# Performance work log

Hardware: AMD Instinct MI355X
Metric: run time of the kernel (lower is better)

Reference implementation:

```python
import jax, jax.numpy as jnp
import numpy as np

B, C, T, F_ = 4, 128, 1000, 65
H, E, Dh = 4, 8, 32          # E = ceil(512/65), Dh = C // H
POOL, STRIDE = 10, 5
EPS = 1e-5


def setup_inputs() -> dict:
    key = jax.random.key(0)
    ks = jax.random.split(key, 16)
    s = 0.05
    d = {}
    d['batch'] = jax.random.normal(ks[0], (B, C, T, F_), jnp.float32)
    d['pos_cond'] = jax.random.normal(ks[1], (B, C, T, F_), jnp.float32)
    d['neg_cond'] = jax.random.normal(ks[2], (B, C, T, F_), jnp.float32)
    # per-head 1x1 conv params (stacked over heads), PReLU slopes, LN4DCF affine
    d['WQ'] = jax.random.normal(ks[3], (H, E, C), jnp.float32) * s
    d['bQ'] = jax.random.normal(ks[4], (H, E), jnp.float32) * s
    d['aQ'] = jnp.full((H,), 0.25, jnp.float32)
    d['gQ'] = jnp.ones((H, E, F_), jnp.float32)
    d['betQ'] = jnp.zeros((H, E, F_), jnp.float32)
    d['WK'] = jax.random.normal(ks[5], (H, E, C), jnp.float32) * s
    d['bK'] = jax.random.normal(ks[6], (H, E), jnp.float32) * s
    d['aK'] = jnp.full((H,), 0.25, jnp.float32)
    d['gK'] = jnp.ones((H, E, F_), jnp.float32)
    d['betK'] = jnp.zeros((H, E, F_), jnp.float32)
    d['WV'] = jax.random.normal(ks[7], (H, Dh, C), jnp.float32) * s
    d['bV'] = jax.random.normal(ks[8], (H, Dh), jnp.float32) * s
    d['aV'] = jnp.full((H,), 0.25, jnp.float32)
    d['gV'] = jnp.ones((H, Dh, F_), jnp.float32)
    d['betV'] = jnp.zeros((H, Dh, F_), jnp.float32)
    d['Wp'] = jax.random.normal(ks[9], (C, C), jnp.float32) * s
    d['bp'] = jax.random.normal(ks[10], (C,), jnp.float32) * s
    d['ap'] = jnp.full((1,), 0.25, jnp.float32)
    d['gp'] = jnp.ones((C, F_), jnp.float32)
    d['betp'] = jnp.zeros((C, F_), jnp.float32)
    return d


def _avg_pool_time(x):
    # x: [B, C, T, F] -> pool along T (torch pools after transposing to [.., F, T])
    xt = jnp.transpose(x, (0, 1, 3, 2))  # [B, C, F, T]
    y = jax.lax.reduce_window(xt, 0.0, jax.lax.add,
                              (1, 1, 1, POOL), (1, 1, 1, STRIDE), 'VALID') / POOL
    return jnp.transpose(y, (0, 1, 3, 2))  # [B, C, T', F]


def _head_branch(x, W, b, a, g, bet):
    # x: [B, Cin, Tx, F]; W: [H, Co, Cin] -> y: [H, B, Co, Tx, F]
    y = jnp.einsum('bctf,hec->hbetf', x, W) + b[:, None, :, None, None]
    y = jnp.where(y >= 0, y, a[:, None, None, None, None] * y)  # PReLU
    mu = jnp.mean(y, axis=(2, 4), keepdims=True)                 # LN over (C, F)
    var = jnp.var(y, axis=(2, 4), keepdims=True)
    return (y - mu) / jnp.sqrt(var + EPS) * g[:, None, :, None, :] + bet[:, None, :, None, :]


def reference(batch, pos_cond, neg_cond,
              WQ, bQ, aQ, gQ, betQ,
              WK, bK, aK, gK, betK,
              WV, bV, aV, gV, betV,
              Wp, bp, ap, gp, betp):
    cond = jnp.concatenate([_avg_pool_time(pos_cond), -_avg_pool_time(neg_cond)], axis=2)
    Tc = cond.shape[2]

    Q = _head_branch(batch, WQ, bQ, aQ, gQ, betQ)   # [H,B,E,T,F]
    K = _head_branch(cond, WK, bK, aK, gK, betK)    # [H,B,E,Tc,F]
    V = _head_branch(cond, WV, bV, aV, gV, betV)    # [H,B,Dh,Tc,F]

    Qf = jnp.transpose(Q, (0, 1, 3, 2, 4)).reshape(H, B, T, E * F_)
    Kf = jnp.transpose(K, (0, 1, 3, 2, 4)).reshape(H, B, Tc, E * F_)
    Vf = jnp.transpose(V, (0, 1, 3, 2, 4)).reshape(H, B, Tc, Dh * F_)

    scale = 1.0 / jnp.sqrt(jnp.float32(E * F_))
    attn = jax.nn.softmax(jnp.einsum('hbtd,hbsd->hbts', Qf, Kf) * scale, axis=-1)
    out = jnp.einsum('hbts,hbse->hbte', attn, Vf)   # [H,B,T,Dh*F]

    out = out.reshape(H, B, T, Dh, F_)
    out = jnp.transpose(out, (1, 0, 3, 2, 4)).reshape(B, C, T, F_)

    # concat projection: conv1x1 + PReLU + LN4DCF over (C, F)
    y = jnp.einsum('bctf,ec->betf', out, Wp) + bp[None, :, None, None]
    y = jnp.where(y >= 0, y, ap[0] * y)
    mu = jnp.mean(y, axis=(1, 3), keepdims=True)
    var = jnp.var(y, axis=(1, 3), keepdims=True)
    y = (y - mu) / jnp.sqrt(var + EPS) * gp[None, :, None, :] + betp[None, :, None, :]
    return y
```

## Files before the change

### kernel.cpp

```cpp
#include <hip/hip_runtime.h>
#include <hip/hip_bf16.h>

typedef unsigned short u16;
typedef __attribute__((ext_vector_type(8))) short bfrag;
typedef __attribute__((ext_vector_type(4))) float f32x4;

#define B_ 4
#define C_ 128
#define T_ 1000
#define F_ 65
#define H_ 4
#define E_ 8
#define DH_ 32
#define TP_ 199
#define TC_ 398
#define DQK 520
#define DQKP 544
#define DV 2080
#define SP_ 416
#define QROWS 1008
#define EPS 1e-5f

__device__ __forceinline__ float bf2f(u16 u) {
    union { float f; unsigned int i; } v; v.i = ((unsigned int)u) << 16; return v.f;
}
__device__ __forceinline__ u16 f2bf(float f) {
    union { float f; unsigned int i; } v; v.f = f;
    unsigned int x = v.i;
    return (u16)((x + 0x7FFFu + ((x >> 16) & 1u)) >> 16);
}

__device__ __forceinline__ float ldx(const float* p, int i) { return p[i]; }
__device__ __forceinline__ float ldx(const u16* p, int i) { return bf2f(p[i]); }

__device__ __forceinline__ float wred_sum(float v) {
#pragma unroll
    for (int o = 32; o > 0; o >>= 1) v += __shfl_down(v, o, 64);
    return __shfl(v, 0, 64);
}

__global__ __launch_bounds__(256)
void pool_kernel(const float* __restrict__ pos, const float* __restrict__ neg,
                 u16* __restrict__ cond) {
    int idx = blockIdx.x * 256 + threadIdx.x;
    const int N = B_ * C_ * TC_ * F_;
    if (idx >= N) return;
    int f  = idx % F_;
    int tc = (idx / F_) % TC_;
    int c  = (idx / (F_ * TC_)) % C_;
    int b  = idx / (F_ * TC_ * C_);
    const float* src; float sign; int t0;
    if (tc < TP_) { src = pos; sign =  1.f; t0 = tc * 5; }
    else          { src = neg; sign = -1.f; t0 = (tc - TP_) * 5; }
    int base = ((b * C_ + c) * T_ + t0) * F_ + f;
    float s = 0.f;
#pragma unroll
    for (int k = 0; k < 10; k++) s += src[base + k * F_];
    cond[idx] = f2bf(s * (sign * 0.1f));
}

template <typename XT>
__global__ __launch_bounds__(256)
void qk_branch_kernel(const XT* __restrict__ x, int Tx, int rowsper, int ldout,
                      const float* __restrict__ W, const float* __restrict__ bias,
                      const float* __restrict__ alpha,
                      const float* __restrict__ g, const float* __restrict__ bet,
                      u16* __restrict__ out) {
    __shared__ float xs[C_ * F_ + 8];
    int b = blockIdx.x / Tx, t = blockIdx.x % Tx;
    int tid = threadIdx.x;
    int xbase = (b * C_) * Tx * F_ + t * F_;
    for (int i = tid; i < C_ * F_; i += 256) {
        int c = i / F_, f = i % F_;
        xs[i] = ldx(x, xbase + c * Tx * F_ + f);
    }
    if (tid < 8) xs[C_ * F_ + tid] = 0.f;
    __syncthreads();

    int row = tid >> 3;
    int oct = tid & 7;
    int h = row >> 3;
    float acc[9];
    float bb = bias[row];
#pragma unroll
    for (int j = 0; j < 9; j++) acc[j] = bb;
    for (int c = 0; c < C_; c++) {
        float w = W[row * C_ + c];
        const float* xr = &xs[c * F_ + oct];
#pragma unroll
        for (int j = 0; j < 9; j++) acc[j] = fmaf(w, xr[8 * j], acc[j]);
    }
    float a = alpha[h];
    float sum = 0.f, ss = 0.f;
#pragma unroll
    for (int j = 0; j < 9; j++) {
        int f = oct + 8 * j;
        if (f < F_) {
            float v = acc[j];
            v = (v >= 0.f) ? v : a * v;
            acc[j] = v;
            sum += v; ss += v * v;
        }
    }
    sum = wred_sum(sum); ss = wred_sum(ss);
    float mu = sum * (1.f / 520.f);
    float var = ss * (1.f / 520.f) - mu * mu;
    float rs = rsqrtf(var + EPS);
    size_t obase = (size_t)((h * B_ + b) * rowsper + t) * ldout + (row & 7) * F_;
#pragma unroll
    for (int j = 0; j < 9; j++) {
        int f = oct + 8 * j;
        if (f < F_) {
            float gv = g[row * F_ + f];
            float bv = bet[row * F_ + f];
            out[obase + f] = f2bf((acc[j] - mu) * rs * gv + bv);
        }
    }
}

__global__ __launch_bounds__(256)
void v_branch_kernel(const u16* __restrict__ x,
                     const float* __restrict__ W, const float* __restrict__ bias,
                     const float* __restrict__ alpha,
                     const float* __restrict__ g, const float* __restrict__ bet,
                     u16* __restrict__ out) {
    __shared__ float xs[C_ * F_ + 1];
    int b = blockIdx.x / TC_, t = blockIdx.x % TC_;
    int tid = threadIdx.x;
    int xbase = (b * C_) * TC_ * F_ + t * F_;
    for (int i = tid; i < C_ * F_; i += 256) {
        int c = i / F_, f = i % F_;
        xs[i] = bf2f(x[xbase + c * TC_ * F_ + f]);
    }
    if (tid == 0) xs[C_ * F_] = 0.f;
    __syncthreads();

    int row = tid >> 1;
    int half = tid & 1;
    int h = row >> 5;
    int f0 = half ? 33 : 0;
    float acc[33];
    float bb = bias[row];
#pragma unroll
    for (int j = 0; j < 33; j++) acc[j] = bb;
    for (int c = 0; c < C_; c++) {
        float w = W[row * C_ + c];
        const float* xr = &xs[c * F_ + f0];
#pragma unroll
        for (int j = 0; j < 33; j++) acc[j] = fmaf(w, xr[j], acc[j]);
    }
    float a = alpha[h];
    float sum = 0.f, ss = 0.f;
#pragma unroll
    for (int j = 0; j < 33; j++) {
        if (f0 + j < F_) {
            float v = acc[j];
            v = (v >= 0.f) ? v : a * v;
            acc[j] = v;
            sum += v; ss += v * v;
        }
    }
    sum = wred_sum(sum); ss = wred_sum(ss);
    float mu = sum * (1.f / 2080.f);
    float var = ss * (1.f / 2080.f) - mu * mu;
    float rs = rsqrtf(var + EPS);
    size_t obase = (size_t)((h * B_ + b) * TC_ + t) * DV + (row & 31) * F_ + f0;
#pragma unroll
    for (int j = 0; j < 33; j++) {
        if (f0 + j < F_) {
            float gv = g[row * F_ + f0 + j];
            float bv = bet[row * F_ + f0 + j];
            out[obase + j] = f2bf((acc[j] - mu) * rs * gv + bv);
        }
    }
}

__global__ __launch_bounds__(256)
void transpose_v_kernel(const u16* __restrict__ Vf, u16* __restrict__ Vt) {
    __shared__ u16 tileb[32][33];
    int id = blockIdx.x;
    int sb = id % 13; id /= 13;
    int eb = id % 65; int hb = id / 65;
    const u16* src = Vf + (size_t)hb * TC_ * DV;
    u16* dst = Vt + (size_t)hb * DV * SP_;
    int j = threadIdx.x & 31, i0 = threadIdx.x >> 5;
#pragma unroll
    for (int k = 0; k < 4; k++) {
        int i = i0 + 8 * k;
        int s = sb * 32 + i, e = eb * 32 + j;
        u16 v = 0;
        if (s < TC_) v = src[(size_t)s * DV + e];
        tileb[i][j] = v;
    }
    __syncthreads();
#pragma unroll
    for (int k = 0; k < 4; k++) {
        int i2 = i0 + 8 * k;
        int e = eb * 32 + i2, s = sb * 32 + j;
        dst[(size_t)e * SP_ + s] = tileb[j][i2];
    }
}

__global__ __launch_bounds__(256, 4)
void attn_kernel(const u16* __restrict__ Qf, const u16* __restrict__ Kf,
                 const u16* __restrict__ Vt, float* __restrict__ out) {
    __shared__ u16 qlds[16 * 552];
    __shared__ u16 plds[16 * 424];
    __shared__ float redmax[16 * 4];
    __shared__ float redsum[16 * 4];

    int tile = blockIdx.x % 63;
    int hb   = blockIdx.x / 63;
    int h = hb >> 2, b = hb & 3;
    int tid = threadIdx.x;
    int wave = tid >> 6, lane = tid & 63;
    int g = lane >> 4;
    int n = lane & 15;
    int tq0 = tile * 16;

    const u16* qbase = Qf + (size_t)(hb * QROWS + tq0) * DQK;
    for (int i = tid; i < 16 * 69; i += 256) {
        int q = i / 69, cb = i % 69;
        uint4 val = make_uint4(0, 0, 0, 0);
        if (cb < 65) val = *(const uint4*)(qbase + (size_t)q * DQK + cb * 8);
        *(uint4*)(&qlds[q * 552 + cb * 8]) = val;
    }
    __syncthreads();

    f32x4 acc[7];
#pragma unroll
    for (int i = 0; i < 7; i++) acc[i] = (f32x4){0.f, 0.f, 0.f, 0.f};
    const u16* kslab = Kf + (size_t)hb * SP_ * DQKP;
    for (int c = 0; c < 17; c++) {
        bfrag aq = *(const bfrag*)(&qlds[n * 552 + c * 32 + g * 8]);
#pragma unroll
        for (int i = 0; i < 7; i++) {
            int tau = wave + 4 * i;
            if (tau < 26) {
                bfrag bk = *(const bfrag*)(kslab + (size_t)(tau * 16 + n) * DQKP + c * 32 + g * 8);
                acc[i] = __builtin_amdgcn_mfma_f32_16x16x32_bf16(aq, bk, acc[i], 0, 0, 0);
            }
        }
    }

    const float scale = 0.043852900965f;
    float m4[4], s4[4];
#pragma unroll
    for (int r = 0; r < 4; r++) {
        float mx = -1e30f;
#pragma unroll
        for (int i = 0; i < 7; i++) {
            int tau = wave + 4 * i;
            int s = tau * 16 + n;
            if (tau < 26 && s < TC_) mx = fmaxf(mx, acc[i][r] * scale);
        }
        mx = fmaxf(mx, __shfl_xor(mx, 1, 64));
        mx = fmaxf(mx, __shfl_xor(mx, 2, 64));
        mx = fmaxf(mx, __shfl_xor(mx, 4, 64));
        mx = fmaxf(mx, __shfl_xor(mx, 8, 64));
        m4[r] = mx;
    }
    if (n == 0) {
#pragma unroll
        for (int r = 0; r < 4; r++) redmax[(g * 4 + r) * 4 + wave] = m4[r];
    }
    __syncthreads();
#pragma unroll
    for (int r = 0; r < 4; r++) {
        int q = g * 4 + r;
        m4[r] = fmaxf(fmaxf(redmax[q * 4 + 0], redmax[q * 4 + 1]),
                      fmaxf(redmax[q * 4 + 2], redmax[q * 4 + 3]));
        s4[r] = 0.f;
    }
#pragma unroll
    for (int i = 0; i < 7; i++) {
        int tau = wave + 4 * i;
        if (tau < 26) {
            int s = tau * 16 + n;
#pragma unroll
            for (int r = 0; r < 4; r++) {
                float e = (s < TC_) ? __expf(acc[i][r] * scale - m4[r]) : 0.f;
                acc[i][r] = e;
                s4[r] += e;
            }
        }
    }
#pragma unroll
    for (int r = 0; r < 4; r++) {
        float sm = s4[r];
        sm += __shfl_xor(sm, 1, 64);
        sm += __shfl_xor(sm, 2, 64);
        sm += __shfl_xor(sm, 4, 64);
        sm += __shfl_xor(sm, 8, 64);
        s4[r] = sm;
    }
    if (n == 0) {
#pragma unroll
        for (int r = 0; r < 4; r++) redsum[(g * 4 + r) * 4 + wave] = s4[r];
    }
    __syncthreads();
#pragma unroll
    for (int r = 0; r < 4; r++) {
        int q = g * 4 + r;
        float tot = redsum[q * 4 + 0] + redsum[q * 4 + 1] + redsum[q * 4 + 2] + redsum[q * 4 + 3];
        s4[r] = 1.0f / tot;
    }
#pragma unroll
    for (int i = 0; i < 7; i++) {
        int tau = wave + 4 * i;
        if (tau < 26) {
            int s = tau * 16 + n;
#pragma unroll
            for (int r = 0; r < 4; r++) {
                plds[(g * 4 + r) * 424 + s] = f2bf(acc[i][r] * s4[r]);
            }
        }
    }
    __syncthreads();

    bfrag bp[13];
#pragma unroll
    for (int c = 0; c < 13; c++)
        bp[c] = *(const bfrag*)(&plds[n * 424 + c * 32 + g * 8]);

    const u16* vslab = Vt + (size_t)hb * DV * SP_;
    int t = tq0 + n;
    for (int j = 0; j < 17; j++) {
        int p = wave + 4 * j;
        if (p >= 65) break;
        int e0 = p * 32;
        f32x4 a0 = (f32x4){0.f, 0.f, 0.f, 0.f};
        f32x4 a1 = (f32x4){0.f, 0.f, 0.f, 0.f};
#pragma unroll
        for (int c = 0; c < 13; c++) {
            bfrag v0 = *(const bfrag*)(vslab + (size_t)(e0 + n) * SP_ + c * 32 + g * 8);
            bfrag v1 = *(const bfrag*)(vslab + (size_t)(e0 + 16 + n) * SP_ + c * 32 + g * 8);
            a0 = __builtin_amdgcn_mfma_f32_16x16x32_bf16(v0, bp[c], a0, 0, 0, 0);
            a1 = __builtin_amdgcn_mfma_f32_16x16x32_bf16(v1, bp[c], a1, 0, 0, 0);
        }
        if (t < T_) {
#pragma unroll
            for (int r = 0; r < 4; r++) {
                int e = e0 + g * 4 + r;
                int dh = e / F_, f = e - dh * F_;
                out[((size_t)(b * C_ + h * DH_ + dh) * T_ + t) * F_ + f] = a0[r];
                int e2 = e0 + 16 + g * 4 + r;
                int dh2 = e2 / F_, f2 = e2 - dh2 * F_;
                out[((size_t)(b * C_ + h * DH_ + dh2) * T_ + t) * F_ + f2] = a1[r];
            }
        }
    }
}

__global__ __launch_bounds__(256)
void wconv_kernel(const float* __restrict__ W, u16* __restrict__ Wbf) {
    int i = blockIdx.x * 256 + threadIdx.x;
    if (i < C_ * C_) Wbf[i] = f2bf(W[i]);
}

__global__ __launch_bounds__(256, 4)
void proj_mfma_kernel(float* __restrict__ io, const u16* __restrict__ Wbf,
                      const float* __restrict__ bpr, const float* __restrict__ apr,
                      const float* __restrict__ gpr, const float* __restrict__ betpr) {
    __shared__ u16 xt[80 * 136];
    __shared__ float wsum[4], wss[4];
    int b = blockIdx.x / T_, t = blockIdx.x % T_;
    int tid = threadIdx.x;
    size_t xbase = (size_t)(b * C_) * T_ * F_ + (size_t)t * F_;

    for (int i = tid; i < C_ * F_; i += 256) {
        int c = i / F_, f = i % F_;
        xt[f * 136 + c] = f2bf(io[xbase + (size_t)c * T_ * F_ + f]);
    }
    for (int i = tid; i < 15 * 128; i += 256) {
        int f = 65 + i / 128, c = i % 128;
        xt[f * 136 + c] = 0;
    }
    __syncthreads();

    int wave = tid >> 6, lane = tid & 63, g = lane >> 4, n = lane & 15;
    f32x4 acc[2][5];
#pragma unroll
    for (int a = 0; a < 2; a++)
#pragma unroll
        for (int ft = 0; ft < 5; ft++) acc[a][ft] = (f32x4){0.f, 0.f, 0.f, 0.f};

    for (int c32 = 0; c32 < 4; c32++) {
        bfrag aw0 = *(const bfrag*)(Wbf + (size_t)(wave * 32 + n) * C_ + c32 * 32 + g * 8);
        bfrag aw1 = *(const bfrag*)(Wbf + (size_t)(wave * 32 + 16 + n) * C_ + c32 * 32 + g * 8);
#pragma unroll
        for (int ft = 0; ft < 5; ft++) {
            bfrag bx = *(const bfrag*)(&xt[(ft * 16 + n) * 136 + c32 * 32 + g * 8]);
            acc[0][ft] = __builtin_amdgcn_mfma_f32_16x16x32_bf16(aw0, bx, acc[0][ft], 0, 0, 0);
            acc[1][ft] = __builtin_amdgcn_mfma_f32_16x16x32_bf16(aw1, bx, acc[1][ft], 0, 0, 0);
        }
    }

    float a_p = apr[0];
    float sum = 0.f, ss = 0.f;
#pragma unroll
    for (int a = 0; a < 2; a++) {
        int e0 = wave * 32 + a * 16 + g * 4;
#pragma unroll
        for (int r = 0; r < 4; r++) {
            float bb = bpr[e0 + r];
#pragma unroll
            for (int ft = 0; ft < 5; ft++) {
                float v = acc[a][ft][r] + bb;
                v = (v >= 0.f) ? v : a_p * v;
                acc[a][ft][r] = v;
                int f = ft * 16 + n;
                if (f < F_) { sum += v; ss += v * v; }
            }
        }
    }
    sum = wred_sum(sum); ss = wred_sum(ss);
    if (lane == 0) { wsum[wave] = sum; wss[wave] = ss; }
    __syncthreads();
    float tsum = wsum[0] + wsum[1] + wsum[2] + wsum[3];
    float tss  = wss[0] + wss[1] + wss[2] + wss[3];
    float mu = tsum * (1.f / 8320.f);
    float var = tss * (1.f / 8320.f) - mu * mu;
    float rs = rsqrtf(var + EPS);

#pragma unroll
    for (int a = 0; a < 2; a++) {
#pragma unroll
        for (int r = 0; r < 4; r++) {
            int e = wave * 32 + a * 16 + g * 4 + r;
#pragma unroll
            for (int ft = 0; ft < 5; ft++) {
                int f = ft * 16 + n;
                if (f < F_) {
                    io[((size_t)(b * C_ + e) * T_ + t) * F_ + f] =
                        (acc[a][ft][r] - mu) * rs * gpr[e * F_ + f] + betpr[e * F_ + f];
                }
            }
        }
    }
}

extern "C" void kernel_launch(void* const* d_in, const int* in_sizes, int n_in,
                              void* d_out, int out_size, void* d_ws, size_t ws_size,
                              hipStream_t stream) {
    const float* batch = (const float*)d_in[0];
    const float* pos   = (const float*)d_in[1];
    const float* neg   = (const float*)d_in[2];
    const float* WQ   = (const float*)d_in[3];
    const float* bQ   = (const float*)d_in[4];
    const float* aQ   = (const float*)d_in[5];
    const float* gQ   = (const float*)d_in[6];
    const float* betQ = (const float*)d_in[7];
    const float* WK   = (const float*)d_in[8];
    const float* bK   = (const float*)d_in[9];
    const float* aK   = (const float*)d_in[10];
    const float* gK   = (const float*)d_in[11];
    const float* betK = (const float*)d_in[12];
    const float* WV   = (const float*)d_in[13];
    const float* bV   = (const float*)d_in[14];
    const float* aV   = (const float*)d_in[15];
    const float* gV   = (const float*)d_in[16];
    const float* betV = (const float*)d_in[17];
    const float* Wp   = (const float*)d_in[18];
    const float* bp   = (const float*)d_in[19];
    const float* ap   = (const float*)d_in[20];
    const float* gp   = (const float*)d_in[21];
    const float* betp = (const float*)d_in[22];

    char* ws = (char*)d_ws;
    u16* Vt   = (u16*)(ws);
    u16* cond = (u16*)(ws);
    u16* Qf   = (u16*)(ws + 27688960);
    u16* Kf   = (u16*)(ws + 44462080);
    u16* Vf   = (u16*)(ws + 51703808);
    u16* Wbf  = (u16*)(ws + 51703808);
    float* o  = (float*)d_out;

    const int NPOOL = B_ * C_ * TC_ * F_;
    pool_kernel<<<(NPOOL + 255) / 256, 256, 0, stream>>>(pos, neg, cond);
    qk_branch_kernel<float><<<B_ * T_,  256, 0, stream>>>(batch, T_,  QROWS, DQK,  WQ, bQ, aQ, gQ, betQ, Qf);
    qk_branch_kernel<u16>  <<<B_ * TC_, 256, 0, stream>>>(cond,  TC_, SP_,   DQKP, WK, bK, aK, gK, betK, Kf);
    v_branch_kernel <<<B_ * TC_, 256, 0, stream>>>(cond, WV, bV, aV, gV, betV, Vf);
    transpose_v_kernel<<<16 * 65 * 13, 256, 0, stream>>>(Vf, Vt);
    wconv_kernel<<<(C_ * C_ + 255) / 256, 256, 0, stream>>>(Wp, Wbf);
    attn_kernel<<<16 * 63, 256, 0, stream>>>(Qf, Kf, Vt, o);
    proj_mfma_kernel<<<B_ * T_, 256, 0, stream>>>(o, Wbf, bp, ap, gp, betp);
}
```

Before: 966.1 us.

## Move Q/K/V branch convolutions to bf16 MFMA with split-precision weights

Replaces the scalar FP32 FMA loops in the Q, K and V per-head 1x1 conv branches with MFMA bf16 matrix ops. To keep accuracy, weights (and, for Q, the fp32 input) are split into bf16 hi/lo parts and the products are summed in extra MFMAs. The projection kernel gets the same hi/lo weight split, which adds MFMA work there. A zero-fill kernel for the padded K buffer and a weight conversion kernel are added, costing extra launches and more traffic.

```diff
diff --git a/kernel.cpp b/kernel.cpp
--- a/kernel.cpp
+++ b/kernel.cpp
@@ -30,13 +30,30 @@
     return (u16)((x + 0x7FFFu + ((x >> 16) & 1u)) >> 16);
 }
 
-__device__ __forceinline__ float ldx(const float* p, int i) { return p[i]; }
-__device__ __forceinline__ float ldx(const u16* p, int i) { return bf2f(p[i]); }
-
 __device__ __forceinline__ float wred_sum(float v) {
 #pragma unroll
     for (int o = 32; o > 0; o >>= 1) v += __shfl_down(v, o, 64);
     return __shfl(v, 0, 64);
+}
+
+__global__ __launch_bounds__(256)
+void zerofill_kernel(uint4* __restrict__ dst, int n16) {
+    int i = blockIdx.x * 256 + threadIdx.x;
+    if (i < n16) dst[i] = make_uint4(0, 0, 0, 0);
+}
+
+__global__ __launch_bounds__(256)
+void wconv3_kernel(const float* __restrict__ WQ, const float* __restrict__ WK,
+                   const float* __restrict__ WV, u16* __restrict__ dst) {
+    int i = blockIdx.x * 256 + threadIdx.x;
+    if (i >= 24576) return;
+    float v; int hipos, lopos;
+    if (i < 4096)      { v = WQ[i];        hipos = i;        lopos = i + 4096;  }
+    else if (i < 8192) { v = WK[i - 4096]; hipos = i + 4096; lopos = i + 8192;  }
+    else               { v = WV[i - 8192]; hipos = i + 8192; lopos = i + 24576; }
+    u16 hi = f2bf(v);
+    dst[hipos] = hi;
+    dst[lopos] = f2bf(v - bf2f(hi));
 }
 
 __global__ __launch_bounds__(256)
@@ -59,118 +76,193 @@
     cond[idx] = f2bf(s * (sign * 0.1f));
 }
 
-template <typename XT>
-__global__ __launch_bounds__(256)
-void qk_branch_kernel(const XT* __restrict__ x, int Tx, int rowsper, int ldout,
-                      const float* __restrict__ W, const float* __restrict__ bias,
-                      const float* __restrict__ alpha,
-                      const float* __restrict__ g, const float* __restrict__ bet,
-                      u16* __restrict__ out) {
-    __shared__ float xs[C_ * F_ + 8];
+template <typename XT, bool SPLITX>
+__global__ __launch_bounds__(256, 4)
+void qk_mfma_kernel(const XT* __restrict__ x, int Tx, int rowsper, int ldout,
+                    const u16* __restrict__ Wbf, const float* __restrict__ bias,
+                    const float* __restrict__ alpha,
+                    const float* __restrict__ g, const float* __restrict__ bet,
+                    u16* __restrict__ out) {
+    constexpr int XLO = 80 * 136;
+    __shared__ u16 xt[(SPLITX ? 2 : 1) * 80 * 136];
+    __shared__ float redS[8], redQ[8];
     int b = blockIdx.x / Tx, t = blockIdx.x % Tx;
     int tid = threadIdx.x;
-    int xbase = (b * C_) * Tx * F_ + t * F_;
+    size_t xbase = (size_t)(b * C_) * Tx * F_ + (size_t)t * F_;
     for (int i = tid; i < C_ * F_; i += 256) {
         int c = i / F_, f = i % F_;
-        xs[i] = ldx(x, xbase + c * Tx * F_ + f);
-    }
-    if (tid < 8) xs[C_ * F_ + tid] = 0.f;
-    __syncthreads();
-
-    int row = tid >> 3;
-    int oct = tid & 7;
-    int h = row >> 3;
-    float acc[9];
-    float bb = bias[row];
-#pragma unroll
-    for (int j = 0; j < 9; j++) acc[j] = bb;
-    for (int c = 0; c < C_; c++) {
-        float w = W[row * C_ + c];
-        const float* xr = &xs[c * F_ + oct];
-#pragma unroll
-        for (int j = 0; j < 9; j++) acc[j] = fmaf(w, xr[8 * j], acc[j]);
-    }
-    float a = alpha[h];
+        if constexpr (SPLITX) {
+            float v = (float)x[xbase + (size_t)c * Tx * F_ + f];
+            u16 hi = f2bf(v);
+            xt[f * 136 + c] = hi;
+            xt[XLO + f * 136 + c] = f2bf(v - bf2f(hi));
+        } else {
+            xt[f * 136 + c] = (u16)x[xbase + (size_t)c * Tx * F_ + f];
+        }
+    }
+    for (int i = tid; i < 15 * 128; i += 256) {
+        xt[(65 + i / 128) * 136 + (i % 128)] = 0;
+        if constexpr (SPLITX) xt[XLO + (65 + i / 128) * 136 + (i % 128)] = 0;
+    }
+    __syncthreads();
+
+    int wave = tid >> 6, lane = tid & 63, gq = lane >> 4, n = lane & 15;
+    int mt = wave & 1, fg = wave >> 1;
+    int ftbase = fg ? 3 : 0;
+    const int nft = 3;
+    int jmax = fg ? 2 : 3;
+    const u16* Wlo = Wbf + 32 * C_;
+    f32x4 acc[3];
+#pragma unroll
+    for (int j = 0; j < nft; j++) acc[j] = (f32x4){0.f, 0.f, 0.f, 0.f};
+
+    for (int c32 = 0; c32 < 4; c32++) {
+        bfrag awh = *(const bfrag*)(Wbf + (size_t)(mt * 16 + n) * C_ + c32 * 32 + gq * 8);
+        bfrag awl = *(const bfrag*)(Wlo + (size_t)(mt * 16 + n) * C_ + c32 * 32 + gq * 8);
+#pragma unroll
+        for (int j = 0; j < nft; j++) {
+            if (j < jmax) {
+                int boff = ((ftbase + j) * 16 + n) * 136 + c32 * 32 + gq * 8;
+                bfrag bxh = *(const bfrag*)(&xt[boff]);
+                acc[j] = __builtin_amdgcn_mfma_f32_16x16x32_bf16(awh, bxh, acc[j], 0, 0, 0);
+                acc[j] = __builtin_amdgcn_mfma_f32_16x16x32_bf16(awl, bxh, acc[j], 0, 0, 0);
+                if constexpr (SPLITX) {
+                    bfrag bxl = *(const bfrag*)(&xt[XLO + boff]);
+                    acc[j] = __builtin_amdgcn_mfma_f32_16x16x32_bf16(awh, bxl, acc[j], 0, 0, 0);
+                }
+            }
+        }
+    }
+
+    int h = mt * 2 + (gq >> 1);
+    int er0 = mt * 16 + gq * 4;
+    float ap = alpha[h];
     float sum = 0.f, ss = 0.f;
 #pragma unroll
-    for (int j = 0; j < 9; j++) {
-        int f = oct + 8 * j;
-        if (f < F_) {
-            float v = acc[j];
-            v = (v >= 0.f) ? v : a * v;
-            acc[j] = v;
-            sum += v; ss += v * v;
-        }
-    }
-    sum = wred_sum(sum); ss = wred_sum(ss);
-    float mu = sum * (1.f / 520.f);
-    float var = ss * (1.f / 520.f) - mu * mu;
+    for (int j = 0; j < nft; j++) {
+        if (j < jmax) {
+#pragma unroll
+            for (int r = 0; r < 4; r++) {
+                float v = acc[j][r] + bias[er0 + r];
+                v = (v >= 0.f) ? v : ap * v;
+                acc[j][r] = v;
+                int f = (ftbase + j) * 16 + n;
+                if (f < F_) { sum += v; ss += v * v; }
+            }
+        }
+    }
+#pragma unroll
+    for (int o = 1; o <= 8; o <<= 1) {
+        sum += __shfl_xor(sum, o, 64);
+        ss  += __shfl_xor(ss, o, 64);
+    }
+    sum += __shfl_xor(sum, 16, 64);
+    ss  += __shfl_xor(ss, 16, 64);
+    if (n == 0 && (gq & 1) == 0) { redS[h * 2 + fg] = sum; redQ[h * 2 + fg] = ss; }
+    __syncthreads();
+    float ts = redS[h * 2 + 0] + redS[h * 2 + 1];
+    float tq = redQ[h * 2 + 0] + redQ[h * 2 + 1];
+    float mu = ts * (1.f / 520.f);
+    float var = tq * (1.f / 520.f) - mu * mu;
     float rs = rsqrtf(var + EPS);
-    size_t obase = (size_t)((h * B_ + b) * rowsper + t) * ldout + (row & 7) * F_;
-#pragma unroll
-    for (int j = 0; j < 9; j++) {
-        int f = oct + 8 * j;
-        if (f < F_) {
-            float gv = g[row * F_ + f];
-            float bv = bet[row * F_ + f];
-            out[obase + f] = f2bf((acc[j] - mu) * rs * gv + bv);
-        }
-    }
-}
-
-__global__ __launch_bounds__(256)
-void v_branch_kernel(const u16* __restrict__ x,
-                     const float* __restrict__ W, const float* __restrict__ bias,
-                     const float* __restrict__ alpha,
-                     const float* __restrict__ g, const float* __restrict__ bet,
-                     u16* __restrict__ out) {
-    __shared__ float xs[C_ * F_ + 1];
+
+    size_t obase = (size_t)((h * B_ + b) * rowsper + t) * ldout;
+#pragma unroll
+    for (int j = 0; j < nft; j++) {
+        if (j < jmax) {
+#pragma unroll
+            for (int r = 0; r < 4; r++) {
+                int f = (ftbase + j) * 16 + n;
+                if (f < F_) {
+                    int er = er0 + r;
+                    int el = er & 7;
+                    out[obase + el * F_ + f] =
+                        f2bf((acc[j][r] - mu) * rs * g[er * F_ + f] + bet[er * F_ + f]);
+                }
+            }
+        }
+    }
+}
+
+__global__ __launch_bounds__(256, 4)
+void v_mfma_kernel(const u16* __restrict__ x, const u16* __restrict__ Wbf,
+                   const float* __restrict__ bias, const float* __restrict__ alpha,
+                   const float* __restrict__ g, const float* __restrict__ bet,
+                   u16* __restrict__ out) {
+    __shared__ u16 xt[80 * 136];
     int b = blockIdx.x / TC_, t = blockIdx.x % TC_;
     int tid = threadIdx.x;
-    int xbase = (b * C_) * TC_ * F_ + t * F_;
+    size_t xbase = (size_t)(b * C_) * TC_ * F_ + (size_t)t * F_;
     for (int i = tid; i < C_ * F_; i += 256) {
         int c = i / F_, f = i % F_;
-        xs[i] = bf2f(x[xbase + c * TC_ * F_ + f]);
-    }
-    if (tid == 0) xs[C_ * F_] = 0.f;
-    __syncthreads();
-
-    int row = tid >> 1;
-    int half = tid & 1;
-    int h = row >> 5;
-    int f0 = half ? 33 : 0;
-    float acc[33];
-    float bb = bias[row];
-#pragma unroll
-    for (int j = 0; j < 33; j++) acc[j] = bb;
-    for (int c = 0; c < C_; c++) {
-        float w = W[row * C_ + c];
-        const float* xr = &xs[c * F_ + f0];
-#pragma unroll
-        for (int j = 0; j < 33; j++) acc[j] = fmaf(w, xr[j], acc[j]);
-    }
-    float a = alpha[h];
+        xt[f * 136 + c] = x[xbase + (size_t)c * TC_ * F_ + f];
+    }
+    for (int i = tid; i < 15 * 128; i += 256)
+        xt[(65 + i / 128) * 136 + (i % 128)] = 0;
+    __syncthreads();
+
+    int wave = tid >> 6, lane = tid & 63, gq = lane >> 4, n = lane & 15;
+    const u16* Wlo = Wbf + 128 * C_;
+    f32x4 acc[2][5];
+#pragma unroll
+    for (int a = 0; a < 2; a++)
+#pragma unroll
+        for (int ft = 0; ft < 5; ft++) acc[a][ft] = (f32x4){0.f, 0.f, 0.f, 0.f};
+
+    for (int c32 = 0; c32 < 4; c32++) {
+        bfrag aw0h = *(const bfrag*)(Wbf + (size_t)(wave * 32 + n) * C_ + c32 * 32 + gq * 8);
+        bfrag aw0l = *(const bfrag*)(Wlo + (size_t)(wave * 32 + n) * C_ + c32 * 32 + gq * 8);
+        bfrag aw1h = *(const bfrag*)(Wbf + (size_t)(wave * 32 + 16 + n) * C_ + c32 * 32 + gq * 8);
+        bfrag aw1l = *(const bfrag*)(Wlo + (size_t)(wave * 32 + 16 + n) * C_ + c32 * 32 + gq * 8);
+#pragma unroll
+        for (int ft = 0; ft < 5; ft++) {
+            bfrag bx = *(const bfrag*)(&xt[(ft * 16 + n) * 136 + c32 * 32 + gq * 8]);
+            acc[0][ft] = __builtin_amdgcn_mfma_f32_16x16x32_bf16(aw0h, bx, acc[0][ft], 0, 0, 0);
+            acc[0][ft] = __builtin_amdgcn_mfma_f32_16x16x32_bf16(aw0l, bx, acc[0][ft], 0, 0, 0);
+            acc[1][ft] = __builtin_amdgcn_mfma_f32_16x16x32_bf16(aw1h, bx, acc[1][ft], 0, 0, 0);
+            acc[1][ft] = __builtin_amdgcn_mfma_f32_16x16x32_bf16(aw1l, bx, acc[1][ft], 0, 0, 0);
+        }
+    }
+
+    int h = wave;
+    float ap = alpha[h];
     float sum = 0.f, ss = 0.f;
 #pragma unroll
-    for (int j = 0; j < 33; j++) {
-        if (f0 + j < F_) {
-            float v = acc[j];
-            v = (v >= 0.f) ? v : a * v;
-            acc[j] = v;
-            sum += v; ss += v * v;
+    for (int a = 0; a < 2; a++) {
+        int er0 = wave * 32 + a * 16 + gq * 4;
+#pragma unroll
+        for (int r = 0; r < 4; r++) {
+            float bb = bias[er0 + r];
+#pragma unroll
+            for (int ft = 0; ft < 5; ft++) {
+                float v = acc[a][ft][r] + bb;
+                v = (v >= 0.f) ? v : ap * v;
+                acc[a][ft][r] = v;
+                int f = ft * 16 + n;
+                if (f < F_) { sum += v; ss += v * v; }
+            }
         }
     }
     sum = wred_sum(sum); ss = wred_sum(ss);
     float mu = sum * (1.f / 2080.f);
     float var = ss * (1.f / 2080.f) - mu * mu;
     float rs = rsqrtf(var + EPS);
-    size_t obase = (size_t)((h * B_ + b) * TC_ + t) * DV + (row & 31) * F_ + f0;
-#pragma unroll
-    for (int j = 0; j < 33; j++) {
-        if (f0 + j < F_) {
-            float gv = g[row * F_ + f0 + j];
-            float bv = bet[row * F_ + f0 + j];
-            out[obase + j] = f2bf((acc[j] - mu) * rs * gv + bv);
+
+    size_t obase = (size_t)((h * B_ + b) * TC_ + t) * DV;
+#pragma unroll
+    for (int a = 0; a < 2; a++) {
+#pragma unroll
+        for (int r = 0; r < 4; r++) {
+            int er = wave * 32 + a * 16 + gq * 4 + r;
+            int drow = er & 31;
+#pragma unroll
+            for (int ft = 0; ft < 5; ft++) {
+                int f = ft * 16 + n;
+                if (f < F_) {
+                    out[obase + drow * F_ + f] =
+                        f2bf((acc[a][ft][r] - mu) * rs * g[er * F_ + f] + bet[er * F_ + f]);
+                }
+            }
         }
     }
 }
@@ -355,7 +447,12 @@
 __global__ __launch_bounds__(256)
 void wconv_kernel(const float* __restrict__ W, u16* __restrict__ Wbf) {
     int i = blockIdx.x * 256 + threadIdx.x;
-    if (i < C_ * C_) Wbf[i] = f2bf(W[i]);
+    if (i < C_ * C_) {
+        float v = W[i];
+        u16 hi = f2bf(v);
+        Wbf[i] = hi;
+        Wbf[C_ * C_ + i] = f2bf(v - bf2f(hi));
+    }
 }
 
 __global__ __launch_bounds__(256, 4)
@@ -379,6 +476,7 @@
     __syncthreads();
 
     int wave = tid >> 6, lane = tid & 63, g = lane >> 4, n = lane & 15;
+    const u16* Wlo = Wbf + C_ * C_;
     f32x4 acc[2][5];
 #pragma unroll
     for (int a = 0; a < 2; a++)
@@ -386,13 +484,17 @@
         for (int ft = 0; ft < 5; ft++) acc[a][ft] = (f32x4){0.f, 0.f, 0.f, 0.f};
 
     for (int c32 = 0; c32 < 4; c32++) {
-        bfrag aw0 = *(const bfrag*)(Wbf + (size_t)(wave * 32 + n) * C_ + c32 * 32 + g * 8);
-        bfrag aw1 = *(const bfrag*)(Wbf + (size_t)(wave * 32 + 16 + n) * C_ + c32 * 32 + g * 8);
+        bfrag aw0h = *(const bfrag*)(Wbf + (size_t)(wave * 32 + n) * C_ + c32 * 32 + g * 8);
+        bfrag aw0l = *(const bfrag*)(Wlo + (size_t)(wave * 32 + n) * C_ + c32 * 32 + g * 8);
+        bfrag aw1h = *(const bfrag*)(Wbf + (size_t)(wave * 32 + 16 + n) * C_ + c32 * 32 + g * 8);
+        bfrag aw1l = *(const bfrag*)(Wlo + (size_t)(wave * 32 + 16 + n) * C_ + c32 * 32 + g * 8);
 #pragma unroll
         for (int ft = 0; ft < 5; ft++) {
             bfrag bx = *(const bfrag*)(&xt[(ft * 16 + n) * 136 + c32 * 32 + g * 8]);
-            acc[0][ft] = __builtin_amdgcn_mfma_f32_16x16x32_bf16(aw0, bx, acc[0][ft], 0, 0, 0);
-            acc[1][ft] = __builtin_amdgcn_mfma_f32_16x16x32_bf16(aw1, bx, acc[1][ft], 0, 0, 0);
+            acc[0][ft] = __builtin_amdgcn_mfma_f32_16x16x32_bf16(aw0h, bx, acc[0][ft], 0, 0, 0);
+            acc[0][ft] = __builtin_amdgcn_mfma_f32_16x16x32_bf16(aw0l, bx, acc[0][ft], 0, 0, 0);
+            acc[1][ft] = __builtin_amdgcn_mfma_f32_16x16x32_bf16(aw1h, bx, acc[1][ft], 0, 0, 0);
+            acc[1][ft] = __builtin_amdgcn_mfma_f32_16x16x32_bf16(aw1l, bx, acc[1][ft], 0, 0, 0);
         }
     }
 
@@ -470,19 +572,26 @@
     char* ws = (char*)d_ws;
     u16* Vt   = (u16*)(ws);
     u16* cond = (u16*)(ws);
+    u16* Wqkv = (u16*)(ws + 26490880);
     u16* Qf   = (u16*)(ws + 27688960);
     u16* Kf   = (u16*)(ws + 44462080);
     u16* Vf   = (u16*)(ws + 51703808);
-    u16* Wbf  = (u16*)(ws + 51703808);
+    u16* Wpbf = (u16*)(ws + 51703808);
+    u16* WQbf = Wqkv;
+    u16* WKbf = Wqkv + 8192;
+    u16* WVbf = Wqkv + 16384;
     float* o  = (float*)d_out;
 
+    wconv3_kernel<<<96, 256, 0, stream>>>(WQ, WK, WV, Wqkv);
     const int NPOOL = B_ * C_ * TC_ * F_;
     pool_kernel<<<(NPOOL + 255) / 256, 256, 0, stream>>>(pos, neg, cond);
-    qk_branch_kernel<float><<<B_ * T_,  256, 0, stream>>>(batch, T_,  QROWS, DQK,  WQ, bQ, aQ, gQ, betQ, Qf);
-    qk_branch_kernel<u16>  <<<B_ * TC_, 256, 0, stream>>>(cond,  TC_, SP_,   DQKP, WK, bK, aK, gK, betK, Kf);
-    v_branch_kernel <<<B_ * TC_, 256, 0, stream>>>(cond, WV, bV, aV, gV, betV, Vf);
+    const int KF16 = (16 * SP_ * DQKP * 2) / 16;
+    zerofill_kernel<<<(KF16 + 255) / 256, 256, 0, stream>>>((uint4*)Kf, KF16);
+    qk_mfma_kernel<float, true><<<B_ * T_,  256, 0, stream>>>(batch, T_,  QROWS, DQK,  WQbf, bQ, aQ, gQ, betQ, Qf);
+    qk_mfma_kernel<u16, false> <<<B_ * TC_, 256, 0, stream>>>(cond,  TC_, SP_,   DQKP, WKbf, bK, aK, gK, betK, Kf);
+    v_mfma_kernel<<<B_ * TC_, 256, 0, stream>>>(cond, WVbf, bV, aV, gV, betV, Vf);
     transpose_v_kernel<<<16 * 65 * 13, 256, 0, stream>>>(Vf, Vt);
-    wconv_kernel<<<(C_ * C_ + 255) / 256, 256, 0, stream>>>(Wp, Wbf);
+    wconv_kernel<<<(C_ * C_ + 255) / 256, 256, 0, stream>>>(Wp, Wpbf);
     attn_kernel<<<16 * 63, 256, 0, stream>>>(Qf, Kf, Vt, o);
-    proj_mfma_kernel<<<B_ * T_, 256, 0, stream>>>(o, Wbf, bp, ap, gp, betp);
-}
+    proj_mfma_kernel<<<B_ * T_, 256, 0, stream>>>(o, Wpbf, bp, ap, gp, betp);
+}
```

Measured after the change: 894.8 us. 1.08x faster.
